# Optimization experiments

Measured on AMD Instinct MI355X. Metric: run time of the kernel, lower is better.

## Reference

```python
import jax, jax.numpy as jnp
import numpy as np

N, E_DIM, T = 32, 512, 2048
N_E = 8192
BETA = 0.25

def setup_inputs() -> dict:
    key = jax.random.key(0)
    k1, k2 = jax.random.split(key)
    z = jax.random.normal(k1, (N, E_DIM, T), dtype=jnp.float32)
    # nn.Embedding weight initialized uniform(-1/n_e, 1/n_e)
    emb = jax.random.uniform(k2, (N_E, E_DIM), dtype=jnp.float32,
                             minval=-1.0 / N_E, maxval=1.0 / N_E)
    return {"z": z, "emb": emb}

def reference(z, emb):
    n, width, t = z.shape
    # preprocess: (N, C, T) -> (N, T, C) -> (N*T, C)
    zf = jnp.transpose(z, (0, 2, 1)).reshape(-1, width)  # [M, e_dim]
    # squared euclidean distances: ||z||^2 + ||e||^2 - 2 z e^T
    d = (jnp.sum(zf ** 2, axis=1, keepdims=True)
         + jnp.sum(emb ** 2, axis=1)
         - 2.0 * jnp.matmul(zf, emb.T))  # [M, n_e]
    idx = jnp.argmin(d, axis=1)  # [M]
    z_q = emb[idx]  # [M, e_dim]
    sg = jax.lax.stop_gradient
    loss = jnp.mean((z_q - sg(zf)) ** 2) + BETA * jnp.mean((sg(z_q) - zf) ** 2)
    # straight-through estimator
    z_q = zf + sg(z_q - zf)
    # (N*T, C) -> (N, T, C) -> (N, C, T)
    z_q = jnp.transpose(z_q.reshape(n, t, width), (0, 2, 1))
    # perplexity from codebook usage histogram
    one_hot = jax.nn.one_hot(idx, emb.shape[0], dtype=zf.dtype)  # [M, n_e]
    e_mean = jnp.mean(one_hot, axis=0)
    perplexity = jnp.exp(-jnp.sum(e_mean * jnp.log(e_mean + 1e-10)))
    return (z_q, loss, perplexity)
```

## Files before the change

### kernel.cpp

```cpp
#include <hip/hip_runtime.h>
#include <stdint.h>

#define NE 8192
#define KD 512
#define MT 65536

typedef __attribute__((ext_vector_type(8))) short bf16x8;
typedef __attribute__((ext_vector_type(4))) float f32x4;

union U128 { uint4 u; bf16x8 b; };

#define WS_SUMZ2   0
#define WS_SUMSMIN 4
#define WS_HIST    8
#define WS_ZEROSZ  40960
#define WS_E2      40960
#define WS_IDX     73728
#define WS_EMB16   335872
#define WS_Z16     8724480

__device__ __forceinline__ unsigned int f2bf(float f) {
    union { float f; unsigned int u; } c; c.f = f;
    return (c.u + 0x7FFFu + ((c.u >> 16) & 1u)) >> 16;
}

__device__ __forceinline__ void load_lds16(const void* g, void* l) {
    __builtin_amdgcn_global_load_lds((const __attribute__((address_space(1))) void*)g,
                                     (__attribute__((address_space(3))) void*)l,
                                     16, 0, 0);
}

__global__ void k_embprep(const float* __restrict__ emb,
                          unsigned short* __restrict__ emb16,
                          float* __restrict__ e2) {
    const int code = blockIdx.x;
    const int lane = threadIdx.x;
    const float4* row = (const float4*)(emb + (size_t)code * KD);
    float4 a = row[lane * 2];
    float4 b = row[lane * 2 + 1];
    float s = a.x*a.x + a.y*a.y + a.z*a.z + a.w*a.w
            + b.x*b.x + b.y*b.y + b.z*b.z + b.w*b.w;
    uint4 o;
    o.x = f2bf(a.x) | (f2bf(a.y) << 16);
    o.y = f2bf(a.z) | (f2bf(a.w) << 16);
    o.z = f2bf(b.x) | (f2bf(b.y) << 16);
    o.w = f2bf(b.z) | (f2bf(b.w) << 16);
    ((uint4*)(emb16 + (size_t)code * KD))[lane] = o;
    #pragma unroll
    for (int off = 32; off; off >>= 1) s += __shfl_down(s, off, 64);
    if (lane == 0) e2[code] = s;
}

__global__ void k_zprep(const float* __restrict__ z,
                        unsigned short* __restrict__ z16,
                        float* __restrict__ sumz2) {
    __shared__ float arr[64][65];
    __shared__ float red[4];
    const int tid = threadIdx.x;
    const int n  = blockIdx.z;
    const int c0 = blockIdx.y * 64;
    const int t0 = blockIdx.x * 64;
    const int tl4 = (tid & 15) * 4;
    const int cw  = tid >> 4;
    const float* base = z + ((size_t)n * KD + c0) * 2048 + t0;
    float s = 0.f;
    #pragma unroll
    for (int u = 0; u < 4; u++) {
        int c = u * 16 + cw;
        float4 v = *(const float4*)(base + (size_t)c * 2048 + tl4);
        arr[c][tl4 + 0] = v.x; arr[c][tl4 + 1] = v.y;
        arr[c][tl4 + 2] = v.z; arr[c][tl4 + 3] = v.w;
        s += v.x*v.x + v.y*v.y + v.z*v.z + v.w*v.w;
    }
    #pragma unroll
    for (int off = 32; off; off >>= 1) s += __shfl_down(s, off, 64);
    if ((tid & 63) == 0) red[tid >> 6] = s;
    __syncthreads();
    if (tid == 0) atomicAdd(sumz2, red[0] + red[1] + red[2] + red[3]);
    #pragma unroll
    for (int iter = 0; iter < 2; iter++) {
        int task = iter * 256 + tid;
        int row = task >> 3;
        int ch  = task & 7;
        float f0 = arr[ch*8+0][row], f1 = arr[ch*8+1][row],
              f2v = arr[ch*8+2][row], f3 = arr[ch*8+3][row],
              f4 = arr[ch*8+4][row], f5 = arr[ch*8+5][row],
              f6 = arr[ch*8+6][row], f7 = arr[ch*8+7][row];
        uint4 o;
        o.x = f2bf(f0) | (f2bf(f1) << 16);
        o.y = f2bf(f2v) | (f2bf(f3) << 16);
        o.z = f2bf(f4) | (f2bf(f5) << 16);
        o.w = f2bf(f6) | (f2bf(f7) << 16);
        *(uint4*)(z16 + ((size_t)(n * 2048 + t0 + row)) * KD + c0 + ch * 8) = o;
    }
}

__global__ __launch_bounds__(512, 2) void k_main(
    const unsigned short* __restrict__ z16,
    const unsigned short* __restrict__ emb16,
    const float* __restrict__ e2,
    int* __restrict__ g_idx,
    int* __restrict__ hist,
    float* __restrict__ sums)
{
    __shared__ __align__(16) unsigned short zt[128 * 512];
    __shared__ __align__(16) unsigned short et[2][256 * 32];

    const int tid  = threadIdx.x;
    const int lane = tid & 63;
    const int w    = tid >> 6;
    const int wm   = w & 1;
    const int wn   = w >> 1;
    const int quad = lane >> 4;
    const int col  = lane & 15;
    const int m0   = blockIdx.x * 128;

    {
        const int r  = tid >> 2;
        const int jb = (tid & 3) << 4;
        const uint4* gz = (const uint4*)(z16 + (size_t)(m0 + r) * KD);
        uint4* zt4w = (uint4*)zt;
        #pragma unroll
        for (int jj = 0; jj < 16; jj++) {
            int j  = jb + jj;
            int js = (j & 56) | ((j ^ r) & 7);
            zt4w[r * 64 + js] = gz[j];
        }
    }

    const int st_nl0 = w * 16 + (lane >> 2);
    const int st_q   = ((lane & 3) - ((st_nl0 >> 1) & 3)) & 3;
    const int st_q8  = st_q * 8;
    unsigned short* st_l0 = &et[0][0] + w * 512 + lane * 8;
    unsigned short* st_l1 = &et[0][0] + 4096 + w * 512 + lane * 8;

    {
        const unsigned short* g0 = emb16 + ((size_t)(st_nl0) << 9) + st_q8;
        const unsigned short* g1 = emb16 + ((size_t)(128 + st_nl0) << 9) + st_q8;
        load_lds16(g0, st_l0);
        load_lds16(g1, st_l1);
    }

    f32x4 acc[4][4];
    #pragma unroll
    for (int mf = 0; mf < 4; mf++)
        #pragma unroll
        for (int nf = 0; nf < 4; nf++)
            acc[mf][nf] = (f32x4){0.f, 0.f, 0.f, 0.f};

    float rbv[4][4]; int rbi[4][4];
    #pragma unroll
    for (int mf = 0; mf < 4; mf++)
        #pragma unroll
        for (int rg = 0; rg < 4; rg++) { rbv[mf][rg] = 3.0e38f; rbi[mf][rg] = 0; }

    int zbase[4], r7[4];
    #pragma unroll
    for (int mf = 0; mf < 4; mf++) {
        int r = wm * 64 + mf * 16 + col;
        zbase[mf] = r * 64;
        r7[mf] = r & 7;
    }
    int bidx[4];
    #pragma unroll
    for (int nf = 0; nf < 4; nf++) {
        int nn = wn * 64 + nf * 16 + col;
        bidx[nf] = nn * 4 + ((quad + (nn >> 1)) & 3);
    }

    const uint4* zt4 = (const uint4*)zt;
    const uint4* et4[2] = { (const uint4*)&et[0][0], (const uint4*)&et[1][0] };

    __syncthreads();

    bf16x8 afp[2][4];
    #pragma unroll
    for (int mf = 0; mf < 4; mf++) {
        U128 u; u.u = zt4[zbase[mf] + (quad ^ r7[mf])];
        afp[0][mf] = u.b;
    }

    #pragma unroll 1
    for (int chunk = 0; chunk < 32; chunk++) {
        float e2v0 = 0.f, e2v1 = 0.f, e2v2 = 0.f, e2v3 = 0.f;
        #pragma unroll
        for (int kk = 0; kk < 16; kk++) {
            const int buf = kk & 1;
            const int nxt = chunk * 16 + kk + 1;
            if (nxt < 512) {
                const int nchunk = nxt >> 4, nkk = nxt & 15, nbuf = nxt & 1;
                const size_t koff = (size_t)nkk * 32 + st_q8;
                const unsigned short* g0 = emb16 + (((size_t)(nchunk * 256 + st_nl0)) << 9) + koff;
                const unsigned short* g1 = emb16 + (((size_t)(nchunk * 256 + 128 + st_nl0)) << 9) + koff;
                load_lds16(g0, st_l0 + nbuf * 8192);
                load_lds16(g1, st_l1 + nbuf * 8192);
            }
            bf16x8 bfv[4];
            #pragma unroll
            for (int nf = 0; nf < 4; nf++) {
                U128 u; u.u = et4[buf][bidx[nf]];
                bfv[nf] = u.b;
            }
            {
                const int kk1 = (kk + 1) & 15;
                const int jhi  = (kk1 * 4) & 56;
                const int jlow = ((kk1 & 1) << 2) | quad;
                #pragma unroll
                for (int mf = 0; mf < 4; mf++) {
                    U128 u; u.u = zt4[zbase[mf] + (jhi | (jlow ^ r7[mf]))];
                    afp[kk1 & 1][mf] = u.b;
                }
            }
            if (kk == 14) {
                const int nbv = chunk * 256 + wn * 64 + col;
                e2v0 = e2[nbv];      e2v1 = e2[nbv + 16];
                e2v2 = e2[nbv + 32]; e2v3 = e2[nbv + 48];
            }
            __builtin_amdgcn_s_setprio(1);
            #pragma unroll
            for (int mf = 0; mf < 4; mf++)
                #pragma unroll
                for (int nf = 0; nf < 4; nf++)
                    acc[mf][nf] = __builtin_amdgcn_mfma_f32_16x16x32_bf16(
                        afp[buf][mf], bfv[nf], acc[mf][nf], 0, 0, 0);
            __builtin_amdgcn_s_setprio(0);
            __syncthreads();
        }
        const int nb = chunk * 256 + wn * 64 + col;
        #pragma unroll
        for (int mf = 0; mf < 4; mf++) {
            #pragma unroll
            for (int rg = 0; rg < 4; rg++) {
                float v0 = fmaf(-2.f, acc[mf][0][rg], e2v0);
                float v1 = fmaf(-2.f, acc[mf][1][rg], e2v1);
                float v2 = fmaf(-2.f, acc[mf][2][rg], e2v2);
                float v3 = fmaf(-2.f, acc[mf][3][rg], e2v3);
                float bv = v0; int bn = 0;
                if (v1 < bv) { bv = v1; bn = 1; }
                if (v2 < bv) { bv = v2; bn = 2; }
                if (v3 < bv) { bv = v3; bn = 3; }
                if (bv < rbv[mf][rg]) { rbv[mf][rg] = bv; rbi[mf][rg] = nb + (bn << 4); }
            }
            #pragma unroll
            for (int nf = 0; nf < 4; nf++)
                acc[mf][nf] = (f32x4){0.f, 0.f, 0.f, 0.f};
        }
    }

    #pragma unroll
    for (int mf = 0; mf < 4; mf++) {
        #pragma unroll
        for (int rg = 0; rg < 4; rg++) {
            float bv = rbv[mf][rg]; int bi = rbi[mf][rg];
            #pragma unroll
            for (int off = 1; off < 16; off <<= 1) {
                float ov = __shfl_xor(bv, off, 64);
                int   oi = __shfl_xor(bi, off, 64);
                if (ov < bv || (ov == bv && oi < bi)) { bv = ov; bi = oi; }
            }
            rbv[mf][rg] = bv; rbi[mf][rg] = bi;
        }
    }

    __syncthreads();
    float* sv = (float*)&et[0][0];
    int*   si = (int*)(sv + 512);
    if (col == 0) {
        #pragma unroll
        for (int mf = 0; mf < 4; mf++)
            #pragma unroll
            for (int rg = 0; rg < 4; rg++) {
                int rl = wm * 64 + mf * 16 + quad * 4 + rg;
                sv[wn * 128 + rl] = rbv[mf][rg];
                si[wn * 128 + rl] = rbi[mf][rg];
            }
    }
    __syncthreads();
    float myv = 0.f;
    if (tid < 128) {
        float bv = sv[tid]; int bi = si[tid];
        #pragma unroll
        for (int wnn = 1; wnn < 4; wnn++) {
            float ov = sv[wnn * 128 + tid]; int oi = si[wnn * 128 + tid];
            if (ov < bv || (ov == bv && oi < bi)) { bv = ov; bi = oi; }
        }
        g_idx[m0 + tid] = bi;
        atomicAdd(&hist[bi], 1);
        myv = bv;
    }
    #pragma unroll
    for (int off = 32; off; off >>= 1) myv += __shfl_down(myv, off, 64);
    if (lane == 0 && w < 2) atomicAdd(&sums[1], myv);
}

__global__ void k_final(const int* __restrict__ hist,
                        const float* __restrict__ sums,
                        float* __restrict__ out_scalars) {
    __shared__ float red[4];
    const int tid = threadIdx.x;
    float s = 0.f;
    for (int i = tid; i < NE; i += 256) {
        float e = (float)hist[i] * (1.0f / 65536.0f);
        s += e * logf(e + 1e-10f);
    }
    #pragma unroll
    for (int off = 32; off; off >>= 1) s += __shfl_down(s, off, 64);
    if ((tid & 63) == 0) red[tid >> 6] = s;
    __syncthreads();
    if (tid == 0) {
        float total = red[0] + red[1] + red[2] + red[3];
        float perp = expf(-total);
        float loss = 1.25f * (sums[0] + sums[1]) / (65536.0f * 512.0f);
        out_scalars[0] = loss;
        out_scalars[1] = perp;
    }
}

__global__ void k_gather(const float* __restrict__ emb,
                         const int* __restrict__ idx,
                         float* __restrict__ out) {
    __shared__ int ids[256];
    const int n  = blockIdx.y;
    const int t0 = blockIdx.x * 256;
    const int tid = threadIdx.x;
    ids[tid] = idx[n * 2048 + t0 + tid];
    __syncthreads();
    const int tq = tid & 63;
    const int cg = tid >> 6;
    const float* e0 = emb + (size_t)ids[tq * 4 + 0] * KD;
    const float* e1 = emb + (size_t)ids[tq * 4 + 1] * KD;
    const float* e2p = emb + (size_t)ids[tq * 4 + 2] * KD;
    const float* e3 = emb + (size_t)ids[tq * 4 + 3] * KD;
    for (int cb = cg * 4; cb < KD; cb += 16) {
        float4 a = *(const float4*)(e0 + cb);
        float4 b = *(const float4*)(e1 + cb);
        float4 c = *(const float4*)(e2p + cb);
        float4 d = *(const float4*)(e3 + cb);
        float* op = out + ((size_t)(n * KD + cb)) * 2048 + t0 + tq * 4;
        float4 o0 = {a.x, b.x, c.x, d.x};
        float4 o1 = {a.y, b.y, c.y, d.y};
        float4 o2 = {a.z, b.z, c.z, d.z};
        float4 o3 = {a.w, b.w, c.w, d.w};
        *(float4*)(op)        = o0;
        *(float4*)(op + 2048) = o1;
        *(float4*)(op + 4096) = o2;
        *(float4*)(op + 6144) = o3;
    }
}

extern "C" void kernel_launch(void* const* d_in, const int* in_sizes, int n_in,
                              void* d_out, int out_size, void* d_ws, size_t ws_size,
                              hipStream_t stream) {
    (void)in_sizes; (void)n_in; (void)out_size; (void)ws_size;
    const float* z   = (const float*)d_in[0];
    const float* emb = (const float*)d_in[1];
    float* out = (float*)d_out;
    char* ws = (char*)d_ws;

    float*          sums  = (float*)(ws + WS_SUMZ2);
    int*            hist  = (int*)(ws + WS_HIST);
    float*          e2    = (float*)(ws + WS_E2);
    int*            g_idx = (int*)(ws + WS_IDX);
    unsigned short* emb16 = (unsigned short*)(ws + WS_EMB16);
    unsigned short* z16   = (unsigned short*)(ws + WS_Z16);

    hipMemsetAsync(ws, 0, WS_ZEROSZ, stream);

    k_embprep<<<NE, 64, 0, stream>>>(emb, emb16, e2);
    k_zprep<<<dim3(32, 8, 32), 256, 0, stream>>>(z, z16, sums);
    k_main<<<512, 512, 0, stream>>>(z16, emb16, e2, g_idx, hist, sums);
    k_final<<<1, 256, 0, stream>>>(hist, sums, out + 33554432);
    k_gather<<<dim3(8, 32), 256, 0, stream>>>(emb, g_idx, out);
}
```

Baseline: 929.0 us.

## Load codebook fragments directly from global into registers, dropping LDS staging

The codebook tile is no longer staged through a double-buffered LDS array with async global-to-LDS loads. Each wave now fetches its B fragments straight from global memory into a register double buffer one k-step ahead. This removes the per-k-step __syncthreads and the LDS traffic for B. In exchange, each code row is read redundantly by the two wm waves, global latency is exposed to the MFMA loop with only one step of prefetch, and the uncoalesced 16-byte row-strided loads depend on L2/L1 hits.

```diff
diff --git a/kernel.cpp b/kernel.cpp
--- a/kernel.cpp
+++ b/kernel.cpp
@@ -22,12 +22,6 @@
 __device__ __forceinline__ unsigned int f2bf(float f) {
     union { float f; unsigned int u; } c; c.f = f;
     return (c.u + 0x7FFFu + ((c.u >> 16) & 1u)) >> 16;
-}
-
-__device__ __forceinline__ void load_lds16(const void* g, void* l) {
-    __builtin_amdgcn_global_load_lds((const __attribute__((address_space(1))) void*)g,
-                                     (__attribute__((address_space(3))) void*)l,
-                                     16, 0, 0);
 }
 
 __global__ void k_embprep(const float* __restrict__ emb,
@@ -104,7 +98,6 @@
     float* __restrict__ sums)
 {
     __shared__ __align__(16) unsigned short zt[128 * 512];
-    __shared__ __align__(16) unsigned short et[2][256 * 32];
 
     const int tid  = threadIdx.x;
     const int lane = tid & 63;
@@ -128,19 +121,6 @@
         }
     }
 
-    const int st_nl0 = w * 16 + (lane >> 2);
-    const int st_q   = ((lane & 3) - ((st_nl0 >> 1) & 3)) & 3;
-    const int st_q8  = st_q * 8;
-    unsigned short* st_l0 = &et[0][0] + w * 512 + lane * 8;
-    unsigned short* st_l1 = &et[0][0] + 4096 + w * 512 + lane * 8;
-
-    {
-        const unsigned short* g0 = emb16 + ((size_t)(st_nl0) << 9) + st_q8;
-        const unsigned short* g1 = emb16 + ((size_t)(128 + st_nl0) << 9) + st_q8;
-        load_lds16(g0, st_l0);
-        load_lds16(g1, st_l1);
-    }
-
     f32x4 acc[4][4];
     #pragma unroll
     for (int mf = 0; mf < 4; mf++)
@@ -161,23 +141,28 @@
         zbase[mf] = r * 64;
         r7[mf] = r & 7;
     }
-    int bidx[4];
-    #pragma unroll
-    for (int nf = 0; nf < 4; nf++) {
-        int nn = wn * 64 + nf * 16 + col;
-        bidx[nf] = nn * 4 + ((quad + (nn >> 1)) & 3);
-    }
+    int bgl[4];
+    #pragma unroll
+    for (int nf = 0; nf < 4; nf++)
+        bgl[nf] = (wn * 64 + nf * 16 + col) * 64 + quad;
 
     const uint4* zt4 = (const uint4*)zt;
-    const uint4* et4[2] = { (const uint4*)&et[0][0], (const uint4*)&et[1][0] };
-
-    __syncthreads();
-
-    bf16x8 afp[2][4];
+
+    __syncthreads();
+
+    bf16x8 afp[2][4], bfp[2][4];
     #pragma unroll
     for (int mf = 0; mf < 4; mf++) {
         U128 u; u.u = zt4[zbase[mf] + (quad ^ r7[mf])];
         afp[0][mf] = u.b;
+    }
+    {
+        const uint4* bsrc = (const uint4*)emb16;
+        #pragma unroll
+        for (int nf = 0; nf < 4; nf++) {
+            U128 u; u.u = bsrc[bgl[nf]];
+            bfp[0][nf] = u.b;
+        }
     }
 
     #pragma unroll 1
@@ -188,18 +173,13 @@
             const int buf = kk & 1;
             const int nxt = chunk * 16 + kk + 1;
             if (nxt < 512) {
-                const int nchunk = nxt >> 4, nkk = nxt & 15, nbuf = nxt & 1;
-                const size_t koff = (size_t)nkk * 32 + st_q8;
-                const unsigned short* g0 = emb16 + (((size_t)(nchunk * 256 + st_nl0)) << 9) + koff;
-                const unsigned short* g1 = emb16 + (((size_t)(nchunk * 256 + 128 + st_nl0)) << 9) + koff;
-                load_lds16(g0, st_l0 + nbuf * 8192);
-                load_lds16(g1, st_l1 + nbuf * 8192);
-            }
-            bf16x8 bfv[4];
-            #pragma unroll
-            for (int nf = 0; nf < 4; nf++) {
-                U128 u; u.u = et4[buf][bidx[nf]];
-                bfv[nf] = u.b;
+                const int nc = nxt >> 4, nk = nxt & 15;
+                const uint4* bsrc = (const uint4*)(emb16 + ((size_t)nc << 17) + nk * 32);
+                #pragma unroll
+                for (int nf = 0; nf < 4; nf++) {
+                    U128 u; u.u = bsrc[bgl[nf]];
+                    bfp[buf ^ 1][nf] = u.b;
+                }
             }
             {
                 const int kk1 = (kk + 1) & 15;
@@ -222,9 +202,8 @@
                 #pragma unroll
                 for (int nf = 0; nf < 4; nf++)
                     acc[mf][nf] = __builtin_amdgcn_mfma_f32_16x16x32_bf16(
-                        afp[buf][mf], bfv[nf], acc[mf][nf], 0, 0, 0);
+                        afp[buf][mf], bfp[buf][nf], acc[mf][nf], 0, 0, 0);
             __builtin_amdgcn_s_setprio(0);
-            __syncthreads();
         }
         const int nb = chunk * 256 + wn * 64 + col;
         #pragma unroll
@@ -263,7 +242,7 @@
     }
 
     __syncthreads();
-    float* sv = (float*)&et[0][0];
+    float* sv = (float*)zt;
     int*   si = (int*)(sv + 512);
     if (col == 0) {
         #pragma unroll
```

After: 1.986 ms. 2.14x slower.
